# Kernel tuning notes

Hardware: AMD Instinct MI355X
Metric: run time of the kernel (lower is better)

## Reference

```python
import jax, jax.numpy as jnp
import numpy as np

N = 8192          # points per cloud
IN_C = 256        # in_channels
OUT_C = 256       # out_channels
SC = IN_C // 4    # shortcut_out_channels
KNN = 32          # neighbors gathered per point
KP = 15           # kernel points (standard KPConv)
RADIUS = 0.12
EXTENT = RADIUS * 2.0 / 2.5   # radius * kp_extent / conv_radius
NEG_SLOPE = 0.1
EPS = 1e-5


def setup_inputs() -> dict:
    key = jax.random.key(0)
    ks = jax.random.split(key, 10)
    src = jax.random.normal(ks[0], (N, IN_C), jnp.float32)
    tgt = jax.random.normal(ks[1], (N, IN_C), jnp.float32)
    src_coords = jax.random.uniform(ks[2], (N, 3), jnp.float32)
    tgt_coords = jax.random.uniform(ks[3], (N, 3), jnp.float32)
    W_in = jax.random.normal(ks[4], (IN_C, SC), jnp.float32) / np.sqrt(IN_C)
    b_in = jnp.zeros((SC,), jnp.float32)
    kernel_pts = jax.random.normal(ks[5], (KP, 3), jnp.float32) * (0.7 * EXTENT)
    W_kp = jax.random.normal(ks[6], (KP, SC, SC), jnp.float32) / np.sqrt(KP * SC)
    W_out = jax.random.normal(ks[7], (SC, OUT_C), jnp.float32) / np.sqrt(SC)
    b_out = jnp.zeros((OUT_C,), jnp.float32)
    gamma = jnp.ones((OUT_C,), jnp.float32)
    beta = jnp.zeros((OUT_C,), jnp.float32)
    return dict(src=src, tgt=tgt, src_coords=src_coords, tgt_coords=tgt_coords,
                W_in=W_in, b_in=b_in, kernel_pts=kernel_pts, W_kp=W_kp,
                W_out=W_out, b_out=b_out, gamma=gamma, beta=beta)


def _one_cloud(x, coords, W_in, b_in, kernel_pts, W_kp, W_out, b_out, gamma, beta):
    # 1x1 conv in: [N, IN_C] -> [N, SC]
    h = x @ W_in + b_in

    # neighbor search: kNN by squared distance, masked to the conv radius
    d2 = jnp.sum((coords[:, None, :] - coords[None, :, :]) ** 2, axis=-1)  # [N, N]
    _, idx = jax.lax.top_k(-d2, KNN)                                       # [N, KNN]
    nb_coords = coords[idx]                                                # [N, KNN, 3]
    rel = nb_coords - coords[:, None, :]                                   # [N, KNN, 3]
    in_range = jnp.sum(rel ** 2, axis=-1) <= RADIUS ** 2                   # [N, KNN]

    # KPConv: linear correlation to kernel points, masked neighbor aggregate
    diff = rel[:, :, None, :] - kernel_pts[None, None, :, :]               # [N, KNN, KP, 3]
    dist = jnp.sqrt(jnp.sum(diff ** 2, axis=-1))                           # [N, KNN, KP]
    infl = jnp.maximum(1.0 - dist / EXTENT, 0.0) * in_range[:, :, None]    # [N, KNN, KP]
    nb_feats = h[idx]                                                      # [N, KNN, SC]
    agg = jnp.einsum('nkp,nkc->npc', infl, nb_feats)                       # [N, KP, SC]
    h = jnp.einsum('npc,pcd->nd', agg, W_kp)                               # [N, SC]

    # 1x1 conv out: [N, SC] -> [N, OUT_C]
    y = h @ W_out + b_out

    # batch norm over points (training-mode statistics) + affine
    mu = jnp.mean(y, axis=0)
    var = jnp.mean((y - mu) ** 2, axis=0)
    y = gamma * (y - mu) * jax.lax.rsqrt(var + EPS) + beta

    # leaky relu
    return jnp.where(y > 0, y, NEG_SLOPE * y)


def reference(src, tgt, src_coords, tgt_coords, W_in, b_in, kernel_pts, W_kp,
              W_out, b_out, gamma, beta):
    params = (W_in, b_in, kernel_pts, W_kp, W_out, b_out, gamma, beta)
    s = _one_cloud(src, src_coords, *params)
    t = _one_cloud(tgt, tgt_coords, *params)
    return (s, t, src_coords, tgt_coords)
```

## Files before the change

### kernel.cpp

```cpp
#include <hip/hip_runtime.h>
#include <stdint.h>

#define NPTS 8192
#define KNN 32
#define KPN 15
#define SCC 64
#define OUTC 256
#define R2F 0.0144f
#define INV_EXT (1.0f/0.096f)
#define SCAP 128
#define COB 32
#define GD 8
#define NCELL (GD*GD*GD)
#define KJ (KPN*SCC)
#define AGP2 1000

typedef float  f32x4  __attribute__((ext_vector_type(4)));
typedef __bf16 bf16x8 __attribute__((ext_vector_type(8)));
typedef __bf16 bf16x4 __attribute__((ext_vector_type(4)));

__device__ __forceinline__ int cell_of(float x) {
  int c = (int)(x * (float)GD);
  return c < 0 ? 0 : (c > GD-1 ? GD-1 : c);
}

__global__ __launch_bounds__(256) void prep_k(
    const float* __restrict__ scd, const float* __restrict__ tcd,
    float* __restrict__ out,
    const float* __restrict__ Wkp, __bf16* __restrict__ WkpT,
    const float* __restrict__ Win, __bf16* __restrict__ WinF)
{
  int b = blockIdx.x, t = threadIdx.x;
  if (b < 192) {
    int i = b*256 + t;
    out[i] = (i < NPTS*3) ? scd[i] : tcd[i - NPTS*3];
  } else if (b < 432) {
    int i = (b - 192)*256 + t;
    int j = i >> 6, d = i & 63;
    WkpT[(size_t)d*KJ + j] = (__bf16)Wkp[i];
  } else {
    int i = (b - 432)*256 + t;
    int j = i & 7, lane = (i >> 3) & 63, cc = i >> 9;
    int kc = cc >> 2, ct = cc & 3;
    int g16 = lane >> 4, p = lane & 15;
    int k = kc*32 + g16*8 + j;
    WinF[i] = (__bf16)Win[(size_t)k*64 + ct*16 + p];
  }
}

__global__ __launch_bounds__(1024) void grid_build(
    const float* __restrict__ cA, const float* __restrict__ cB,
    unsigned int* __restrict__ starts,
    unsigned int* __restrict__ cursor,
    float* __restrict__ stats)
{
  __shared__ unsigned int hcnt[2][NCELL];
  __shared__ unsigned int a[NCELL], b[NCELL];
  int t = threadIdx.x;
  if (t < NCELL) { hcnt[0][t] = 0u; hcnt[1][t] = 0u; }
  stats[t] = 0.f;
  __syncthreads();
  for (int i = t; i < 2*NPTS; i += 1024) {
    int cloud = i >> 13, n = i & 8191;
    const float* coords = cloud ? cB : cA;
    int cx = cell_of(coords[(size_t)n*3]);
    int cy = cell_of(coords[(size_t)n*3+1]);
    int cz = cell_of(coords[(size_t)n*3+2]);
    atomicAdd(&hcnt[cloud][(cz*GD + cy)*GD + cx], 1u);
  }
  __syncthreads();
  for (int cloud = 0; cloud < 2; ++cloud) {
    if (t < NCELL) a[t] = hcnt[cloud][t];
    __syncthreads();
    unsigned int *s = a, *d = b;
    for (int off = 1; off < NCELL; off <<= 1) {
      if (t < NCELL) {
        unsigned int x = s[t];
        if (t >= off) x += s[t - off];
        d[t] = x;
      }
      __syncthreads();
      unsigned int* tmp = s; s = d; d = tmp;
    }
    if (t < NCELL) {
      unsigned int inc = s[t];
      unsigned int exc = inc - hcnt[cloud][t];
      starts[cloud*520 + t] = exc;
      cursor[cloud*NCELL + t] = exc;
      if (t == NCELL-1) starts[cloud*520 + NCELL] = inc;
    }
    __syncthreads();
  }
}

__global__ __launch_bounds__(256) void grid_scatter(
    const float* __restrict__ cA, const float* __restrict__ cB,
    unsigned int* __restrict__ cursor, float4* __restrict__ sorted,
    float4* __restrict__ coords4)
{
  int i = blockIdx.x*256 + threadIdx.x;
  int cloud = i >> 13, n = i & 8191;
  const float* coords = cloud ? cB : cA;
  float x = coords[(size_t)n*3], y = coords[(size_t)n*3+1], z = coords[(size_t)n*3+2];
  coords4[(size_t)cloud*NPTS + n] = make_float4(x, y, z, 0.f);
  int cell = (cell_of(z)*GD + cell_of(y))*GD + cell_of(x);
  unsigned int slot = atomicAdd(&cursor[cloud*NCELL + cell], 1u);
  sorted[(size_t)cloud*NPTS + slot] = make_float4(x, y, z, __int_as_float(n));
}

__global__ __launch_bounds__(256) void knn_convin_k(
    const float4* __restrict__ coords4,
    const unsigned int* __restrict__ starts, const float4* __restrict__ sorted,
    short* __restrict__ fidx,
    const float* __restrict__ src, const float* __restrict__ tgt,
    const __bf16* __restrict__ WinF, const float* __restrict__ bin,
    __bf16* __restrict__ h)
{
  __shared__ unsigned long long surv[4][SCAP];
  int bId = blockIdx.x;
  int t = threadIdx.x, w = t >> 6, lane = t & 63;
  if (bId < 256) {
    int rt = bId*4 + w;
    int row0 = rt*16;
    const float* x = (row0 >> 13) ? tgt : src;
    int n0 = row0 & 8191;
    int g16 = lane >> 4, p = lane & 15;
    const float* xrow = x + (size_t)(n0 + p)*256;
    f32x4 acc[4];
    #pragma unroll
    for (int ct = 0; ct < 4; ++ct) {
      float bb = bin[ct*16 + p];
      acc[ct] = (f32x4){bb, bb, bb, bb};
    }
    #pragma unroll
    for (int kc = 0; kc < 8; ++kc) {
      float4 xa = *(const float4*)(xrow + kc*32 + g16*8);
      float4 xb = *(const float4*)(xrow + kc*32 + g16*8 + 4);
      bf16x8 af;
      af[0]=(__bf16)xa.x; af[1]=(__bf16)xa.y; af[2]=(__bf16)xa.z; af[3]=(__bf16)xa.w;
      af[4]=(__bf16)xb.x; af[5]=(__bf16)xb.y; af[6]=(__bf16)xb.z; af[7]=(__bf16)xb.w;
      #pragma unroll
      for (int ct = 0; ct < 4; ++ct) {
        bf16x8 bf = *(const bf16x8*)(WinF + (size_t)(kc*4 + ct)*512 + lane*8);
        acc[ct] = __builtin_amdgcn_mfma_f32_16x16x32_bf16(af, bf, acc[ct], 0,0,0);
      }
    }
    #pragma unroll
    for (int r = 0; r < 4; ++r) {
      bf16x4 o;
      o[0] = (__bf16)acc[0][r]; o[1] = (__bf16)acc[1][r];
      o[2] = (__bf16)acc[2][r]; o[3] = (__bf16)acc[3][r];
      *(bf16x4*)(h + (size_t)(row0 + g16*4 + r)*SCC + p*4) = o;
    }
    return;
  }
  int q = (bId - 256)*4 + w;
  int cloud = q >> 13, n = q & 8191;
  float4 qc = coords4[(size_t)cloud*NPTS + n];
  float qx = qc.x, qy = qc.y, qz = qc.z;
  int cx = cell_of(qx), cy = cell_of(qy), cz = cell_of(qz);
  const unsigned int* st = starts + cloud*520;
  const float4* sp = sorted + (size_t)cloud*NPTS;
  int c0 = cx > 0 ? cx-1 : 0;
  int c1 = cx < GD-1 ? cx+1 : GD-1;
  unsigned int cnt = 0;
  for (int dz = -1; dz <= 1; ++dz) {
    int zz = cz + dz; if (zz < 0 || zz > GD-1) continue;
    for (int dy = -1; dy <= 1; ++dy) {
      int yy = cy + dy; if (yy < 0 || yy > GD-1) continue;
      int rb = (zz*GD + yy)*GD;
      unsigned int s = st[rb + c0];
      unsigned int e = st[rb + c1 + 1];
      for (unsigned int jj = s; jj < e; jj += 64) {
        unsigned int j = jj + lane;
        bool keep = false; float d2 = 0.f; unsigned int oi = 0;
        if (j < e) {
          float4 p4 = sp[j];
          float dx = qx-p4.x, dyy = qy-p4.y, dzz = qz-p4.z;
          d2 = fmaf(dx, dx, fmaf(dyy, dyy, dzz*dzz));
          oi = __float_as_uint(p4.w);
          keep = (d2 <= R2F);
        }
        unsigned long long m = __ballot(keep);
        if (keep) {
          unsigned int before = __builtin_amdgcn_mbcnt_hi(
              (unsigned int)(m >> 32),
              __builtin_amdgcn_mbcnt_lo((unsigned int)m, 0u));
          unsigned int pos = cnt + before;
          if (pos < SCAP)
            surv[w][pos] = ((unsigned long long)__float_as_uint(d2) << 32) | oi;
        }
        cnt += (unsigned int)__popcll(m);
      }
    }
  }
  int C = (int)cnt; if (C > SCAP) C = SCAP;
  unsigned long long k0 = (lane      < C) ? surv[w][lane]      : ~0ULL;
  unsigned long long k1 = (lane + 64 < C) ? surv[w][lane + 64] : ~0ULL;
  int r0 = 0, r1 = 0;
  for (int j = 0; j < C; ++j) {
    unsigned long long kj = surv[w][j];
    r0 += (kj < k0);
    r1 += (kj < k1);
  }
  size_t g = (size_t)cloud*NPTS + n;
  if (k0 != ~0ULL && r0 < KNN) fidx[g*KNN + r0] = (short)(k0 & 0xffffu);
  if (k1 != ~0ULL && r1 < KNN) fidx[g*KNN + r1] = (short)(k1 & 0xffffu);
  if (lane >= C && lane < KNN) fidx[g*KNN + lane] = (short)-1;
}

__global__ __launch_bounds__(512, 4) void kpconv_fused(
    const float4* __restrict__ coords4, const float4* __restrict__ sorted,
    const float* __restrict__ kpts, const short* __restrict__ fidx,
    const __bf16* __restrict__ h, const __bf16* __restrict__ WkpT,
    float* __restrict__ h2)
{
  __shared__ __bf16 agg_s[16][AGP2];
  __shared__ float  red2[4*16*17];
  __shared__ int    oidx_s[16];
  int t = threadIdx.x;
  int w = t >> 6, lane = t & 63;
  int b = blockIdx.x;
  int cloud = b >> 9;
  int sbase = (b & 511)*16;
  const float4* c4 = coords4 + (size_t)cloud*NPTS;
  const float4* sp = sorted + (size_t)cloud*NPTS;
  int g16 = lane >> 4;
  int p   = lane & 15;
  int pc  = p < KPN ? p : 0;
  float kpx = kpts[pc*3], kpy = kpts[pc*3+1], kpz = kpts[pc*3+2];
  bf16x8 afrag[2];
  int idxs[2][8];
  int orig[2];
  #pragma unroll
  for (int hf = 0; hf < 2; ++hf) {
    int lp = w*2 + hf;
    float4 se = sp[sbase + lp];
    int o = (int)__float_as_uint(se.w);
    orig[hf] = o;
    if (lane == 0) oidx_s[lp] = o;
    int idxreg = fidx[((size_t)cloud*NPTS + o)*KNN + (lane & 31)];
    float qx = se.x, qy = se.y, qz = se.z;
    #pragma unroll
    for (int j = 0; j < 8; ++j) {
      int k = g16*8 + j;
      int idx = __shfl(idxreg, k);
      idxs[hf][j] = idx < 0 ? 0 : idx;
      float4 nc = c4[idxs[hf][j]];
      float wv = 0.f;
      if (idx >= 0 && p < KPN) {
        float dx = (nc.x - qx) - kpx;
        float dy = (nc.y - qy) - kpy;
        float dz = (nc.z - qz) - kpz;
        float d = sqrtf(fmaf(dx, dx, fmaf(dy, dy, dz*dz)));
        wv = fmaxf(1.0f - d*INV_EXT, 0.0f);
      }
      afrag[hf][j] = (__bf16)wv;
    }
  }
  #pragma unroll
  for (int hf = 0; hf < 2; ++hf) {
    bf16x8 bfrag0, bfrag1, bfrag2, bfrag3;
    #pragma unroll
    for (int j = 0; j < 8; ++j) {
      bf16x4 hv = *(const bf16x4*)(h + ((size_t)cloud*NPTS + idxs[hf][j])*SCC + p*4);
      bfrag0[j] = hv[0]; bfrag1[j] = hv[1]; bfrag2[j] = hv[2]; bfrag3[j] = hv[3];
    }
    f32x4 a0 = {0.f,0.f,0.f,0.f}, a1 = a0, a2 = a0, a3 = a0;
    a0 = __builtin_amdgcn_mfma_f32_16x16x32_bf16(afrag[hf], bfrag0, a0, 0,0,0);
    a1 = __builtin_amdgcn_mfma_f32_16x16x32_bf16(afrag[hf], bfrag1, a1, 0,0,0);
    a2 = __builtin_amdgcn_mfma_f32_16x16x32_bf16(afrag[hf], bfrag2, a2, 0,0,0);
    a3 = __builtin_amdgcn_mfma_f32_16x16x32_bf16(afrag[hf], bfrag3, a3, 0,0,0);
    int lp = w*2 + hf;
    #pragma unroll
    for (int r = 0; r < 4; ++r) {
      int pp = g16*4 + r;
      if (pp < KPN) {
        agg_s[lp][pp*SCC +      p] = (__bf16)a0[r];
        agg_s[lp][pp*SCC + 16 + p] = (__bf16)a1[r];
        agg_s[lp][pp*SCC + 32 + p] = (__bf16)a2[r];
        agg_s[lp][pp*SCC + 48 + p] = (__bf16)a3[r];
      }
    }
  }
  __syncthreads();
  if (w < 4) {
    int dt = w;
    const __bf16* arow = WkpT + (size_t)(dt*16 + p)*KJ + g16*8;
    const __bf16* brow = &agg_s[p][g16*8];
    f32x4 accB = {0.f,0.f,0.f,0.f};
    #pragma unroll
    for (int s = 0; s < 30; ++s) {
      bf16x8 af  = *(const bf16x8*)(arow + s*32);
      bf16x8 bfr = *(const bf16x8*)(brow + s*32);
      accB = __builtin_amdgcn_mfma_f32_16x16x32_bf16(af, bfr, accB, 0, 0, 0);
    }
    #pragma unroll
    for (int r = 0; r < 4; ++r)
      red2[(dt*16 + g16*4 + r)*17 + p] = accB[r];
  }
  __syncthreads();
  #pragma unroll
  for (int e = t; e < 1024; e += 512) {
    int pt = e >> 6, d = e & 63;
    float v = red2[((d >> 4)*16 + (d & 15))*17 + pt];
    h2[((size_t)cloud*NPTS + oidx_s[pt])*SCC + d] = v;
  }
}

__global__ __launch_bounds__(512) void conv_out_bn(
    const float* __restrict__ h2, const float* __restrict__ W,
    const float* __restrict__ b, float* __restrict__ y,
    float* __restrict__ stats)
{
  __shared__ float w_s[SCC*OUTC];
  __shared__ float h_s[COB][SCC];
  __shared__ float rs_s[2][OUTC];
  __shared__ float rs2_s[2][OUTC];
  int t = threadIdx.x;
  int d = t & 255, rg = t >> 8;
  int row0 = blockIdx.x*COB;
  int cloud = (int)(blockIdx.x >> 8);
  {
    const float4* gw = (const float4*)W;
    float4* lw = (float4*)w_s;
    #pragma unroll
    for (int i = 0; i < 8; ++i) lw[t + 512*i] = gw[t + 512*i];
    const float4* gh = (const float4*)(h2 + (size_t)row0*SCC);
    ((float4*)h_s)[t] = gh[t];
  }
  __syncthreads();
  float acc[16];
  float bb = b[d];
  #pragma unroll
  for (int r = 0; r < 16; ++r) acc[r] = bb;
  int rb = rg*16;
  #pragma unroll 4
  for (int c4 = 0; c4 < 16; ++c4) {
    float w0 = w_s[(c4*4+0)*OUTC + d];
    float w1 = w_s[(c4*4+1)*OUTC + d];
    float w2 = w_s[(c4*4+2)*OUTC + d];
    float w3 = w_s[(c4*4+3)*OUTC + d];
    #pragma unroll
    for (int r = 0; r < 16; ++r) {
      float4 hv = *(const float4*)&h_s[rb + r][c4*4];
      acc[r] = fmaf(hv.x,w0, fmaf(hv.y,w1, fmaf(hv.z,w2, fmaf(hv.w,w3, acc[r]))));
    }
  }
  float s = 0.f, s2 = 0.f;
  #pragma unroll
  for (int r = 0; r < 16; ++r) {
    float v = acc[r];
    y[((size_t)row0 + rb + r)*OUTC + d] = v;
    s += v; s2 = fmaf(v, v, s2);
  }
  rs_s[rg][d] = s; rs2_s[rg][d] = s2;
  __syncthreads();
  if (rg == 0) {
    atomicAdd(&stats[cloud*512 + d],       s  + rs_s[1][d]);
    atomicAdd(&stats[cloud*512 + 256 + d], s2 + rs2_s[1][d]);
  }
}

__global__ __launch_bounds__(256) void bn_apply_k(
    float* __restrict__ y, const float* __restrict__ stats,
    const float* __restrict__ gamma, const float* __restrict__ beta)
{
  size_t e = (size_t)blockIdx.x*256 + threadIdx.x;
  int c = (int)(e & 255);
  int cloud = (int)(e >> 21);
  float s  = stats[cloud*512 + c];
  float s2 = stats[cloud*512 + 256 + c];
  float mu  = s * (1.0f/NPTS);
  float var = fmaxf(s2 * (1.0f/NPTS) - mu*mu, 0.f);
  float sc = gamma[c] * rsqrtf(var + 1e-5f);
  float sh = beta[c] - mu*sc;
  float v = fmaf(y[e], sc, sh);
  v = v > 0.f ? v : 0.1f*v;
  y[e] = v;
}

extern "C" void kernel_launch(void* const* d_in, const int* in_sizes, int n_in,
                              void* d_out, int out_size, void* d_ws, size_t ws_size,
                              hipStream_t stream)
{
  (void)in_sizes; (void)n_in; (void)out_size; (void)ws_size;
  const float* src   = (const float*)d_in[0];
  const float* tgt   = (const float*)d_in[1];
  const float* scd   = (const float*)d_in[2];
  const float* tcd   = (const float*)d_in[3];
  const float* W_in  = (const float*)d_in[4];
  const float* b_in  = (const float*)d_in[5];
  const float* kpts  = (const float*)d_in[6];
  const float* W_kp  = (const float*)d_in[7];
  const float* W_out = (const float*)d_in[8];
  const float* b_out = (const float*)d_in[9];
  const float* gamma = (const float*)d_in[10];
  const float* beta  = (const float*)d_in[11];

  char* ws = (char*)d_ws;
  __bf16* h    = (__bf16*)ws;
  float* h2    = (float*)(ws + (4u<<20));
  short* fidx  = (short*)(ws + (8u<<20));
  float* stats = (float*)(ws + (9u<<20));
  __bf16* WkpT = (__bf16*)(ws + (9u<<20) + (64u<<10));
  __bf16* WinF = (__bf16*)(ws + (9u<<20) + (256u<<10));
  float4* coords4 = (float4*)(ws + (9u<<20) + (512u<<10));
  float4* sorted  = (float4*)(ws + (10u<<20));
  unsigned int* starts = (unsigned int*)(ws + (10u<<20) + (512u<<10));
  unsigned int* cursor = (unsigned int*)(ws + (10u<<20) + (520u<<10));

  float* yout = (float*)d_out;

  prep_k<<<496, 256, 0, stream>>>(scd, tcd, yout + (size_t)2*NPTS*OUTC,
                                  W_kp, WkpT, W_in, WinF);
  grid_build<<<1, 1024, 0, stream>>>(scd, tcd, starts, cursor, stats);
  grid_scatter<<<64, 256, 0, stream>>>(scd, tcd, cursor, sorted, coords4);
  knn_convin_k<<<4352, 256, 0, stream>>>(coords4, starts, sorted, fidx,
                                         src, tgt, WinF, b_in, h);
  kpconv_fused<<<1024, 512, 0, stream>>>(coords4, sorted, kpts, fidx, h, WkpT, h2);
  conv_out_bn<<<512, 512, 0, stream>>>(h2, W_out, b_out, yout, stats);
  bn_apply_k<<<16384, 256, 0, stream>>>(yout, stats, gamma, beta);
}
```

Before: 195.9 us.

## Use bf16 MFMA for conv-out, merge grid build into prep, vectorize BN

The output 1x1 conv becomes a bf16 MFMA kernel. h2 is now stored as bf16 and W_out is pre-swizzled into MFMA fragment layout inside the prep kernel. The single-block grid_build kernel is folded into prep_k as an extra block, which saves one launch. The BN apply kernel now processes float4s per thread. Together these aim to cut conv-out FLOP cost, launch overhead and memory traffic, at the cost of bf16 rounding of h2 and W_out.

```diff
diff --git a/kernel.cpp b/kernel.cpp
--- a/kernel.cpp
+++ b/kernel.cpp
@@ -9,7 +9,6 @@
 #define R2F 0.0144f
 #define INV_EXT (1.0f/0.096f)
 #define SCAP 128
-#define COB 32
 #define GD 8
 #define NCELL (GD*GD*GD)
 #define KJ (KPN*SCC)
@@ -24,72 +23,74 @@
   return c < 0 ? 0 : (c > GD-1 ? GD-1 : c);
 }
 
-__global__ __launch_bounds__(256) void prep_k(
+__global__ __launch_bounds__(1024) void prep_k(
     const float* __restrict__ scd, const float* __restrict__ tcd,
     float* __restrict__ out,
     const float* __restrict__ Wkp, __bf16* __restrict__ WkpT,
-    const float* __restrict__ Win, __bf16* __restrict__ WinF)
-{
+    const float* __restrict__ Win, __bf16* __restrict__ WinF,
+    const float* __restrict__ Wout, __bf16* __restrict__ WoutF,
+    unsigned int* __restrict__ starts, unsigned int* __restrict__ cursor,
+    float* __restrict__ stats)
+{
+  __shared__ unsigned int hcnt[2][NCELL];
+  __shared__ unsigned int sa[NCELL], sb[NCELL];
   int b = blockIdx.x, t = threadIdx.x;
-  if (b < 192) {
-    int i = b*256 + t;
+  if (b < 48) {
+    int i = b*1024 + t;
     out[i] = (i < NPTS*3) ? scd[i] : tcd[i - NPTS*3];
-  } else if (b < 432) {
-    int i = (b - 192)*256 + t;
+  } else if (b < 108) {
+    int i = (b - 48)*1024 + t;
     int j = i >> 6, d = i & 63;
     WkpT[(size_t)d*KJ + j] = (__bf16)Wkp[i];
-  } else {
-    int i = (b - 432)*256 + t;
+  } else if (b < 124) {
+    int i = (b - 108)*1024 + t;
     int j = i & 7, lane = (i >> 3) & 63, cc = i >> 9;
     int kc = cc >> 2, ct = cc & 3;
     int g16 = lane >> 4, p = lane & 15;
     int k = kc*32 + g16*8 + j;
     WinF[i] = (__bf16)Win[(size_t)k*64 + ct*16 + p];
-  }
-}
-
-__global__ __launch_bounds__(1024) void grid_build(
-    const float* __restrict__ cA, const float* __restrict__ cB,
-    unsigned int* __restrict__ starts,
-    unsigned int* __restrict__ cursor,
-    float* __restrict__ stats)
-{
-  __shared__ unsigned int hcnt[2][NCELL];
-  __shared__ unsigned int a[NCELL], b[NCELL];
-  int t = threadIdx.x;
-  if (t < NCELL) { hcnt[0][t] = 0u; hcnt[1][t] = 0u; }
-  stats[t] = 0.f;
-  __syncthreads();
-  for (int i = t; i < 2*NPTS; i += 1024) {
-    int cloud = i >> 13, n = i & 8191;
-    const float* coords = cloud ? cB : cA;
-    int cx = cell_of(coords[(size_t)n*3]);
-    int cy = cell_of(coords[(size_t)n*3+1]);
-    int cz = cell_of(coords[(size_t)n*3+2]);
-    atomicAdd(&hcnt[cloud][(cz*GD + cy)*GD + cx], 1u);
-  }
-  __syncthreads();
-  for (int cloud = 0; cloud < 2; ++cloud) {
-    if (t < NCELL) a[t] = hcnt[cloud][t];
+  } else if (b < 156) {
+    int i = (b - 124)*1024 + t;
+    int j = i & 7, lane = (i >> 3) & 63, cc = i >> 9;
+    int kc = cc >> 4, ct = cc & 15;
+    int g16 = lane >> 4, p = lane & 15;
+    int k = kc*32 + g16*8 + j;
+    WoutF[i] = (__bf16)Wout[(size_t)k*256 + ct*16 + p];
+  } else {
+    if (t < NCELL) { hcnt[0][t] = 0u; hcnt[1][t] = 0u; }
+    stats[t] = 0.f;
     __syncthreads();
-    unsigned int *s = a, *d = b;
-    for (int off = 1; off < NCELL; off <<= 1) {
+    for (int i = t; i < 2*NPTS; i += 1024) {
+      int cloud = i >> 13, n = i & 8191;
+      const float* coords = cloud ? tcd : scd;
+      int cx = cell_of(coords[(size_t)n*3]);
+      int cy = cell_of(coords[(size_t)n*3+1]);
+      int cz = cell_of(coords[(size_t)n*3+2]);
+      atomicAdd(&hcnt[cloud][(cz*GD + cy)*GD + cx], 1u);
+    }
+    __syncthreads();
+    for (int cloud = 0; cloud < 2; ++cloud) {
+      if (t < NCELL) sa[t] = hcnt[cloud][t];
+      __syncthreads();
+      unsigned int *s = sa, *d = sb;
+      for (int off = 1; off < NCELL; off <<= 1) {
+        if (t < NCELL) {
+          unsigned int x = s[t];
+          if (t >= off) x += s[t - off];
+          d[t] = x;
+        }
+        __syncthreads();
+        unsigned int* tmp = s; s = d; d = tmp;
+      }
       if (t < NCELL) {
-        unsigned int x = s[t];
-        if (t >= off) x += s[t - off];
-        d[t] = x;
+        unsigned int inc = s[t];
+        unsigned int exc = inc - hcnt[cloud][t];
+        starts[cloud*520 + t] = exc;
+        cursor[cloud*NCELL + t] = exc;
+        if (t == NCELL-1) starts[cloud*520 + NCELL] = inc;
       }
       __syncthreads();
-      unsigned int* tmp = s; s = d; d = tmp;
-    }
-    if (t < NCELL) {
-      unsigned int inc = s[t];
-      unsigned int exc = inc - hcnt[cloud][t];
-      starts[cloud*520 + t] = exc;
-      cursor[cloud*NCELL + t] = exc;
-      if (t == NCELL-1) starts[cloud*520 + NCELL] = inc;
-    }
-    __syncthreads();
+    }
   }
 }
 
@@ -213,7 +214,7 @@
     const float4* __restrict__ coords4, const float4* __restrict__ sorted,
     const float* __restrict__ kpts, const short* __restrict__ fidx,
     const __bf16* __restrict__ h, const __bf16* __restrict__ WkpT,
-    float* __restrict__ h2)
+    __bf16* __restrict__ h2)
 {
   __shared__ __bf16 agg_s[16][AGP2];
   __shared__ float  red2[4*16*17];
@@ -231,13 +232,11 @@
   float kpx = kpts[pc*3], kpy = kpts[pc*3+1], kpz = kpts[pc*3+2];
   bf16x8 afrag[2];
   int idxs[2][8];
-  int orig[2];
   #pragma unroll
   for (int hf = 0; hf < 2; ++hf) {
     int lp = w*2 + hf;
     float4 se = sp[sbase + lp];
     int o = (int)__float_as_uint(se.w);
-    orig[hf] = o;
     if (lane == 0) oidx_s[lp] = o;
     int idxreg = fidx[((size_t)cloud*NPTS + o)*KNN + (lane & 31)];
     float qx = se.x, qy = se.y, qz = se.z;
@@ -304,61 +303,57 @@
   for (int e = t; e < 1024; e += 512) {
     int pt = e >> 6, d = e & 63;
     float v = red2[((d >> 4)*16 + (d & 15))*17 + pt];
-    h2[((size_t)cloud*NPTS + oidx_s[pt])*SCC + d] = v;
-  }
-}
-
-__global__ __launch_bounds__(512) void conv_out_bn(
-    const float* __restrict__ h2, const float* __restrict__ W,
+    h2[((size_t)cloud*NPTS + oidx_s[pt])*SCC + d] = (__bf16)v;
+  }
+}
+
+__global__ __launch_bounds__(256, 2) void conv_out_bn(
+    const __bf16* __restrict__ h2, const __bf16* __restrict__ WoutF,
     const float* __restrict__ b, float* __restrict__ y,
     float* __restrict__ stats)
 {
-  __shared__ float w_s[SCC*OUTC];
-  __shared__ float h_s[COB][SCC];
-  __shared__ float rs_s[2][OUTC];
-  __shared__ float rs2_s[2][OUTC];
-  int t = threadIdx.x;
-  int d = t & 255, rg = t >> 8;
-  int row0 = blockIdx.x*COB;
-  int cloud = (int)(blockIdx.x >> 8);
-  {
-    const float4* gw = (const float4*)W;
-    float4* lw = (float4*)w_s;
-    #pragma unroll
-    for (int i = 0; i < 8; ++i) lw[t + 512*i] = gw[t + 512*i];
-    const float4* gh = (const float4*)(h2 + (size_t)row0*SCC);
-    ((float4*)h_s)[t] = gh[t];
+  __shared__ float rs_s[4][OUTC];
+  __shared__ float rs2_s[4][OUTC];
+  int t = threadIdx.x, w = t >> 6, lane = t & 63;
+  int g16 = lane >> 4, p = lane & 15;
+  int rt = blockIdx.x*4 + w;
+  int row0 = rt*16;
+  int cloud = blockIdx.x >> 7;
+  const __bf16* arow = h2 + (size_t)(row0 + p)*SCC;
+  f32x4 acc[16];
+  #pragma unroll
+  for (int ct = 0; ct < 16; ++ct) {
+    float bb = b[ct*16 + p];
+    acc[ct] = (f32x4){bb, bb, bb, bb};
+  }
+  #pragma unroll
+  for (int kc = 0; kc < 2; ++kc) {
+    bf16x8 af = *(const bf16x8*)(arow + kc*32 + g16*8);
+    #pragma unroll
+    for (int ct = 0; ct < 16; ++ct) {
+      bf16x8 bf = *(const bf16x8*)(WoutF + (size_t)(kc*16 + ct)*512 + lane*8);
+      acc[ct] = __builtin_amdgcn_mfma_f32_16x16x32_bf16(af, bf, acc[ct], 0,0,0);
+    }
+  }
+  #pragma unroll
+  for (int ct = 0; ct < 16; ++ct) {
+    float s = 0.f, s2 = 0.f;
+    #pragma unroll
+    for (int r = 0; r < 4; ++r) {
+      float v = acc[ct][r];
+      y[((size_t)row0 + g16*4 + r)*OUTC + ct*16 + p] = v;
+      s += v; s2 = fmaf(v, v, s2);
+    }
+    s  += __shfl_xor(s, 16);  s  += __shfl_xor(s, 32);
+    s2 += __shfl_xor(s2, 16); s2 += __shfl_xor(s2, 32);
+    if (g16 == 0) { rs_s[w][ct*16 + p] = s; rs2_s[w][ct*16 + p] = s2; }
   }
   __syncthreads();
-  float acc[16];
-  float bb = b[d];
-  #pragma unroll
-  for (int r = 0; r < 16; ++r) acc[r] = bb;
-  int rb = rg*16;
-  #pragma unroll 4
-  for (int c4 = 0; c4 < 16; ++c4) {
-    float w0 = w_s[(c4*4+0)*OUTC + d];
-    float w1 = w_s[(c4*4+1)*OUTC + d];
-    float w2 = w_s[(c4*4+2)*OUTC + d];
-    float w3 = w_s[(c4*4+3)*OUTC + d];
-    #pragma unroll
-    for (int r = 0; r < 16; ++r) {
-      float4 hv = *(const float4*)&h_s[rb + r][c4*4];
-      acc[r] = fmaf(hv.x,w0, fmaf(hv.y,w1, fmaf(hv.z,w2, fmaf(hv.w,w3, acc[r]))));
-    }
-  }
-  float s = 0.f, s2 = 0.f;
-  #pragma unroll
-  for (int r = 0; r < 16; ++r) {
-    float v = acc[r];
-    y[((size_t)row0 + rb + r)*OUTC + d] = v;
-    s += v; s2 = fmaf(v, v, s2);
-  }
-  rs_s[rg][d] = s; rs2_s[rg][d] = s2;
-  __syncthreads();
-  if (rg == 0) {
-    atomicAdd(&stats[cloud*512 + d],       s  + rs_s[1][d]);
-    atomicAdd(&stats[cloud*512 + 256 + d], s2 + rs2_s[1][d]);
+  if (t < 256) {
+    float S  = rs_s[0][t]  + rs_s[1][t]  + rs_s[2][t]  + rs_s[3][t];
+    float S2 = rs2_s[0][t] + rs2_s[1][t] + rs2_s[2][t] + rs2_s[3][t];
+    atomicAdd(&stats[cloud*512 + t],       S);
+    atomicAdd(&stats[cloud*512 + 256 + t], S2);
   }
 }
 
@@ -366,18 +361,25 @@
     float* __restrict__ y, const float* __restrict__ stats,
     const float* __restrict__ gamma, const float* __restrict__ beta)
 {
-  size_t e = (size_t)blockIdx.x*256 + threadIdx.x;
-  int c = (int)(e & 255);
-  int cloud = (int)(e >> 21);
-  float s  = stats[cloud*512 + c];
-  float s2 = stats[cloud*512 + 256 + c];
-  float mu  = s * (1.0f/NPTS);
-  float var = fmaxf(s2 * (1.0f/NPTS) - mu*mu, 0.f);
-  float sc = gamma[c] * rsqrtf(var + 1e-5f);
-  float sh = beta[c] - mu*sc;
-  float v = fmaf(y[e], sc, sh);
-  v = v > 0.f ? v : 0.1f*v;
-  y[e] = v;
+  size_t i = (size_t)blockIdx.x*256 + threadIdx.x;
+  size_t e4 = i*4;
+  int c0 = (int)(e4 & 255);
+  int cloud = (int)(e4 >> 21);
+  float4 v = *(float4*)&y[e4];
+  float vv[4] = {v.x, v.y, v.z, v.w};
+  #pragma unroll
+  for (int k = 0; k < 4; ++k) {
+    int c = c0 + k;
+    float s  = stats[cloud*512 + c];
+    float s2 = stats[cloud*512 + 256 + c];
+    float mu  = s * (1.0f/NPTS);
+    float var = fmaxf(s2 * (1.0f/NPTS) - mu*mu, 0.f);
+    float sc = gamma[c] * rsqrtf(var + 1e-5f);
+    float sh = beta[c] - mu*sc;
+    float o = fmaf(vv[k], sc, sh);
+    vv[k] = o > 0.f ? o : 0.1f*o;
+  }
+  *(float4*)&y[e4] = make_float4(vv[0], vv[1], vv[2], vv[3]);
 }
 
 extern "C" void kernel_launch(void* const* d_in, const int* in_sizes, int n_in,
@@ -400,11 +402,12 @@
 
   char* ws = (char*)d_ws;
   __bf16* h    = (__bf16*)ws;
-  float* h2    = (float*)(ws + (4u<<20));
+  __bf16* h2   = (__bf16*)(ws + (4u<<20));
   short* fidx  = (short*)(ws + (8u<<20));
   float* stats = (float*)(ws + (9u<<20));
   __bf16* WkpT = (__bf16*)(ws + (9u<<20) + (64u<<10));
   __bf16* WinF = (__bf16*)(ws + (9u<<20) + (256u<<10));
+  __bf16* WoutF = (__bf16*)(ws + (9u<<20) + (320u<<10));
   float4* coords4 = (float4*)(ws + (9u<<20) + (512u<<10));
   float4* sorted  = (float4*)(ws + (10u<<20));
   unsigned int* starts = (unsigned int*)(ws + (10u<<20) + (512u<<10));
@@ -412,13 +415,13 @@
 
   float* yout = (float*)d_out;
 
-  prep_k<<<496, 256, 0, stream>>>(scd, tcd, yout + (size_t)2*NPTS*OUTC,
-                                  W_kp, WkpT, W_in, WinF);
-  grid_build<<<1, 1024, 0, stream>>>(scd, tcd, starts, cursor, stats);
+  prep_k<<<157, 1024, 0, stream>>>(scd, tcd, yout + (size_t)2*NPTS*OUTC,
+                                   W_kp, WkpT, W_in, WinF, W_out, WoutF,
+                                   starts, cursor, stats);
   grid_scatter<<<64, 256, 0, stream>>>(scd, tcd, cursor, sorted, coords4);
   knn_convin_k<<<4352, 256, 0, stream>>>(coords4, starts, sorted, fidx,
                                          src, tgt, WinF, b_in, h);
   kpconv_fused<<<1024, 512, 0, stream>>>(coords4, sorted, kpts, fidx, h, WkpT, h2);
-  conv_out_bn<<<512, 512, 0, stream>>>(h2, W_out, b_out, yout, stats);
-  bn_apply_k<<<16384, 256, 0, stream>>>(yout, stats, gamma, beta);
-}
+  conv_out_bn<<<256, 256, 0, stream>>>(h2, WoutF, b_out, yout, stats);
+  bn_apply_k<<<4096, 256, 0, stream>>>(yout, stats, gamma, beta);
+}
```

Result: faster. 174.6 us (-10.8%).
